# Kernel tuning notes

Measured on AMD Instinct MI355X. Metric: run time of the kernel, lower is better.

## Reference

```python
import jax, jax.numpy as jnp
import numpy as np

H = 8
D_MODEL = 1024
D_K = D_MODEL // H
NEG = -1000000000.0


def layer_norm(x, a, b, eps=1e-06):
    # torch std: unbiased (ddof=1); module divides by (std + eps)
    mean = jnp.mean(x, axis=-1, keepdims=True)
    var = jnp.sum((x - mean) ** 2, axis=-1, keepdims=True) / (x.shape[-1] - 1)
    std = jnp.sqrt(var)
    return a * (x - mean) / (std + eps) + b


def setup_inputs() -> dict:
    key = jax.random.key(0)
    ks = jax.random.split(key, 12)
    B, S, D = 8, 1024, D_MODEL
    inp = {
        "query": jax.random.normal(ks[0], (B, S, D), jnp.float32),
        "value": jax.random.normal(ks[1], (B, S, D), jnp.float32),
        "key": jax.random.normal(ks[2], (B, S, D), jnp.float32),
        "mask": jax.random.randint(ks[3], (B, S), 0, 2, jnp.int32),
        "ln_a": jnp.ones((D,), jnp.float32),
        "ln_b": jnp.zeros((D,), jnp.float32),
        "wq": jax.random.normal(ks[4], (D, D), jnp.float32) * 0.02,
        "bq": jnp.zeros((D,), jnp.float32),
        "wk": jax.random.normal(ks[5], (D, D), jnp.float32) * 0.02,
        "bk": jnp.zeros((D,), jnp.float32),
        "wv": jax.random.normal(ks[6], (D, D), jnp.float32) * 0.02,
        "bv": jnp.zeros((D,), jnp.float32),
        "w_aoa": jax.random.normal(ks[7], (2 * D, 2 * D), jnp.float32) * 0.02,  # [out, in]
        "b_aoa": jnp.zeros((2 * D,), jnp.float32),
    }
    return inp


def reference(query, value, key, mask, ln_a, ln_b, wq, bq, wk, bk, wv, bv, w_aoa, b_aoa):
    B, S, D = query.shape
    # mask [B,S] -> [B,1,1,S]
    m = mask[:, None, None, :]
    # norm_q
    q = layer_norm(query, ln_a, ln_b)
    # QKV projections, split heads -> [B,H,S,Dk]
    def split_heads(x):
        return x.reshape(B, -1, H, D_K).transpose(0, 2, 1, 3)
    q_ = split_heads(q @ wq.T + bq)
    k_ = split_heads(key @ wk.T + bk)
    v_ = split_heads(value @ wv.T + bv)
    scores = jnp.einsum("bhqd,bhkd->bhqk", q_, k_) / jnp.sqrt(jnp.float32(D_K))
    scores = jnp.where(m == 0, NEG, scores)
    p = jax.nn.softmax(scores, axis=-1)
    x = jnp.einsum("bhqk,bhkd->bhqd", p, v_)
    x = x.transpose(0, 2, 1, 3).reshape(B, S, D)
    # AoA: concat with (normed) query, linear to 2D, GLU
    z = jnp.concatenate([x, q], axis=-1) @ w_aoa.T + b_aoa
    a, g = jnp.split(z, 2, axis=-1)
    return a * jax.nn.sigmoid(g)
```

## Files before the change

### kernel.cpp

```cpp
#include <hip/hip_runtime.h>

typedef __attribute__((ext_vector_type(8))) __bf16 bf16x8;
typedef __attribute__((ext_vector_type(4))) float f32x4;

__device__ __forceinline__ ushort f2b(float f) {
    uint u = __builtin_bit_cast(uint, f);
    u += 0x7fffu + ((u >> 16) & 1u);
    return (ushort)(u >> 16);
}
__device__ __forceinline__ float b2f(ushort h) {
    uint u = ((uint)h) << 16;
    return __builtin_bit_cast(float, u);
}

__global__ __launch_bounds__(256) void cast_kernel(const float* __restrict__ src,
                                                   ushort* __restrict__ dst) {
    size_t i = ((size_t)blockIdx.x * 256 + threadIdx.x) * 4;
    float4 v = *(const float4*)(src + i);
    ushort4 o;
    o.x = f2b(v.x); o.y = f2b(v.y); o.z = f2b(v.z); o.w = f2b(v.w);
    *(ushort4*)(dst + i) = o;
}

__global__ __launch_bounds__(256) void cast_permute_aoa(const float* __restrict__ src,
                                                        ushort* __restrict__ dst) {
    int n1 = blockIdx.x >> 1;
    int c = (blockIdx.x & 1) * 1024 + threadIdx.x * 4;
    int q = ((n1 & 63) | ((n1 >> 7) << 6)) + ((n1 >> 6) & 1) * 1024;
    float4 v = *(const float4*)(src + (size_t)q * 2048 + c);
    ushort4 o;
    o.x = f2b(v.x); o.y = f2b(v.y); o.z = f2b(v.z); o.w = f2b(v.w);
    *(ushort4*)(dst + (size_t)n1 * 2048 + c) = o;
}

__global__ __launch_bounds__(256) void ln_kernel(const float* __restrict__ x,
                                                 const float* __restrict__ ga,
                                                 const float* __restrict__ be,
                                                 ushort* __restrict__ xq) {
    const int row = blockIdx.x, tid = threadIdx.x;
    __shared__ float red[4];
    float4 v = ((const float4*)(x + (size_t)row * 1024))[tid];
    float sm = v.x + v.y + v.z + v.w;
    for (int off = 32; off; off >>= 1) sm += __shfl_xor(sm, off);
    if ((tid & 63) == 0) red[tid >> 6] = sm;
    __syncthreads();
    float mean = (red[0] + red[1] + red[2] + red[3]) * (1.f / 1024.f);
    __syncthreads();
    float dx = v.x - mean, dy = v.y - mean, dz = v.z - mean, dw = v.w - mean;
    float s2 = dx * dx + dy * dy + dz * dz + dw * dw;
    for (int off = 32; off; off >>= 1) s2 += __shfl_xor(s2, off);
    if ((tid & 63) == 0) red[tid >> 6] = s2;
    __syncthreads();
    float var = (red[0] + red[1] + red[2] + red[3]) * (1.f / 1023.f);
    float inv = 1.f / (sqrtf(var) + 1e-6f);
    float4 g = ((const float4*)ga)[tid];
    float4 bb = ((const float4*)be)[tid];
    ushort4 o;
    o.x = f2b(g.x * dx * inv + bb.x);
    o.y = f2b(g.y * dy * inv + bb.y);
    o.z = f2b(g.z * dz * inv + bb.z);
    o.w = f2b(g.w * dw * inv + bb.w);
    *(ushort4*)&xq[(size_t)row * 2048 + 1024 + tid * 4] = o;
}

template <int MODE>
__global__ __launch_bounds__(512, 2) void gemm6(const ushort* __restrict__ Aq, int ldaq,
                                                const ushort* __restrict__ Ak,
                                                const ushort* __restrict__ Av,
                                                const ushort* __restrict__ B, int ldb,
                                                const float* __restrict__ bias0,
                                                const float* __restrict__ bias1,
                                                const float* __restrict__ bias2,
                                                void* __restrict__ out0,
                                                void* __restrict__ out1,
                                                void* __restrict__ out2,
                                                int K, int NB, float qscale) {
    __shared__ ushort lds[2][32768];

    const int tid = threadIdx.x;
    const int w = tid >> 6, l = tid & 63;
    const int wr = w >> 2, wcn = w & 3;
    const int r16 = l & 15, g4 = l >> 4;

    const int bid = blockIdx.x;
    const int cpx = gridDim.x >> 3;
    const int swz = (bid & 7) * cpx + (bid >> 3);
    const int m0 = (swz / NB) * 256;
    const int n0 = (swz % NB) * 256;

    const int region = (MODE == 0) ? (n0 >> 10) : 0;
    const ushort* A = (MODE == 0) ? (region == 0 ? Aq : (region == 1 ? Ak : Av)) : Aq;
    const int lda = (MODE == 0) ? (region == 0 ? ldaq : 1024) : ldaq;

    const int srow8 = l >> 3;
    const int sxor8 = ((l & 7) ^ srow8) * 8;
    const ushort* As0 = A + (size_t)(m0 + w * 8 + srow8) * lda + sxor8;
    const ushort* Bs0 = B + (size_t)(n0 + w * 8 + srow8) * ldb + sxor8;

    f32x4 acc[8][4];
#pragma unroll
    for (int i = 0; i < 8; i++)
#pragma unroll
        for (int j = 0; j < 4; j++) acc[i][j] = (f32x4){0.f, 0.f, 0.f, 0.f};

    const int sw16 = (r16 & 7) << 4;
    char* ldsb = (char*)&lds[0][0];

#define STAGE_H(sel_, HS_, kt_)                                                            \
    do {                                                                                   \
        const int mat_ = (HS_)&1, half_ = (HS_) >> 1;                                      \
        const ushort* sb_ = mat_ ? Bs0 : As0;                                              \
        const int ld_ = mat_ ? ldb : lda;                                                  \
        _Pragma("unroll") for (int li_ = 0; li_ < 2; li_++) {                              \
            const ushort* src_ = sb_ + (size_t)(half_ * 128 + li_ * 64) * ld_ + (kt_)*64;  \
            int dst_ = (sel_)*65536 + mat_ * 32768 + half_ * 16384 + li_ * 8192 + w * 1024;\
            __builtin_amdgcn_global_load_lds(                                              \
                (const __attribute__((address_space(1))) void*)src_,                       \
                (__attribute__((address_space(3))) void*)(ldsb + dst_), 16, 0, 0);         \
        }                                                                                  \
    } while (0)

    auto LDA4 = [&](bf16x8 (&dst)[4][2], int sel, int half) {
#pragma unroll
        for (int ai = 0; ai < 4; ai++)
#pragma unroll
            for (int ks = 0; ks < 2; ks++)
                dst[ai][ks] = *(const bf16x8*)(ldsb + sel * 65536 + half * 16384 +
                                               (wr * 16 + 32 * ai + r16) * 128 +
                                               ((ks * 64 + g4 * 16) ^ sw16));
    };
    auto LDB2 = [&](bf16x8 (&dst)[2][2], int sel, int half) {
#pragma unroll
        for (int bi = 0; bi < 2; bi++)
#pragma unroll
            for (int ks = 0; ks < 2; ks++)
                dst[bi][ks] = *(const bf16x8*)(ldsb + sel * 65536 + 32768 + half * 16384 +
                                               (wcn * 16 + 64 * bi + r16) * 128 +
                                               ((ks * 64 + g4 * 16) ^ sw16));
    };
    auto MM = [&](bf16x8 (&af)[4][2], bf16x8 (&bf)[2][2], int A0, int B0) {
        __builtin_amdgcn_s_setprio(1);
#pragma unroll
        for (int ks = 0; ks < 2; ks++)
#pragma unroll
            for (int ai = 0; ai < 4; ai++)
#pragma unroll
                for (int bi = 0; bi < 2; bi++)
                    acc[A0 + ai][B0 + bi] = __builtin_amdgcn_mfma_f32_16x16x32_bf16(
                        af[ai][ks], bf[bi][ks], acc[A0 + ai][B0 + bi], 0, 0, 0);
        __builtin_amdgcn_s_setprio(0);
    };

    const int NT = K >> 6;

    STAGE_H(0, 0, 0); STAGE_H(0, 1, 0); STAGE_H(0, 2, 0); STAGE_H(0, 3, 0);
    STAGE_H(1, 0, 1); STAGE_H(1, 1, 1); STAGE_H(1, 2, 1);
    asm volatile("s_waitcnt vmcnt(10)" ::: "memory");
    __builtin_amdgcn_s_barrier();

    bf16x8 aL[4][2], aH[4][2], bL[2][2], bH[2][2];

    for (int t = 0; t < NT - 2; ++t) {
        const int sel = t & 1;
        LDA4(aL, sel, 0); LDB2(bL, sel, 0);
        STAGE_H(sel ^ 1, 3, t + 1);
        __builtin_amdgcn_s_barrier();
        MM(aL, bL, 0, 0);
        asm volatile("s_waitcnt vmcnt(10)" ::: "memory");
        __builtin_amdgcn_s_barrier();
        LDA4(aH, sel, 1);
        STAGE_H(sel, 0, t + 2);
        __builtin_amdgcn_s_barrier();
        MM(aH, bL, 4, 0);
        asm volatile("s_waitcnt vmcnt(10)" ::: "memory");
        __builtin_amdgcn_s_barrier();
        LDB2(bH, sel, 1);
        STAGE_H(sel, 1, t + 2);
        __builtin_amdgcn_s_barrier();
        MM(aH, bH, 4, 2);
        __builtin_amdgcn_s_barrier();
        STAGE_H(sel, 2, t + 2);
        __builtin_amdgcn_s_barrier();
        MM(aL, bH, 0, 2);
        asm volatile("s_waitcnt vmcnt(10)" ::: "memory");
        __builtin_amdgcn_s_barrier();
    }
    {
        const int sel = (NT - 2) & 1;
        LDA4(aL, sel, 0); LDB2(bL, sel, 0);
        STAGE_H(sel ^ 1, 3, NT - 1);
        __builtin_amdgcn_s_barrier();
        MM(aL, bL, 0, 0);
        asm volatile("s_waitcnt vmcnt(10)" ::: "memory");
        __builtin_amdgcn_s_barrier();
        LDA4(aH, sel, 1);
        __builtin_amdgcn_s_barrier();
        MM(aH, bL, 4, 0);
        asm volatile("s_waitcnt vmcnt(8)" ::: "memory");
        __builtin_amdgcn_s_barrier();
        LDB2(bH, sel, 1);
        __builtin_amdgcn_s_barrier();
        MM(aH, bH, 4, 2);
        __builtin_amdgcn_s_barrier();
        MM(aL, bH, 0, 2);
        asm volatile("s_waitcnt vmcnt(4)" ::: "memory");
        __builtin_amdgcn_s_barrier();
    }
    {
        const int sel = (NT - 1) & 1;
        LDA4(aL, sel, 0); LDB2(bL, sel, 0);
        __builtin_amdgcn_s_barrier();
        MM(aL, bL, 0, 0);
        asm volatile("s_waitcnt vmcnt(2)" ::: "memory");
        __builtin_amdgcn_s_barrier();
        LDA4(aH, sel, 1);
        __builtin_amdgcn_s_barrier();
        MM(aH, bL, 4, 0);
        asm volatile("s_waitcnt vmcnt(0)" ::: "memory");
        __builtin_amdgcn_s_barrier();
        LDB2(bH, sel, 1);
        MM(aH, bH, 4, 2);
        MM(aL, bH, 0, 2);
    }
#undef STAGE_H

    if (MODE == 1) {
        float* out = (float*)out0;
#pragma unroll
        for (int bp = 0; bp < 2; bp++) {
            int j = (n0 >> 1) + wcn * 16 + 64 * bp + r16;
            float bsa = bias0[j];
            float bsg = bias0[j + 1024];
#pragma unroll
            for (int a_ = 0; a_ < 8; a_++) {
                int mr = m0 + wr * 16 + 32 * a_ + g4 * 4;
#pragma unroll
                for (int r = 0; r < 4; r++) {
                    float av = acc[a_][2 * bp][r] + bsa;
                    float gv = acc[a_][2 * bp + 1][r] + bsg;
                    out[(size_t)(mr + r) * 1024 + j] = av * (1.f / (1.f + __expf(-gv)));
                }
            }
        }
    } else {
        const int nr0 = n0 & 1023;
        const float* bias = region == 0 ? bias0 : (region == 1 ? bias1 : bias2);
        const float scale = region == 0 ? qscale : 1.f;
        if (region < 2) {
            ushort* C = (ushort*)(region == 0 ? out0 : out1);
#pragma unroll
            for (int b_ = 0; b_ < 4; b_++) {
                int n = nr0 + wcn * 16 + 64 * b_ + r16;
                float bs = bias[n];
#pragma unroll
                for (int a_ = 0; a_ < 8; a_++) {
                    int mr = m0 + wr * 16 + 32 * a_ + g4 * 4;
#pragma unroll
                    for (int r = 0; r < 4; r++)
                        C[(size_t)(mr + r) * 1024 + n] = f2b((acc[a_][b_][r] + bs) * scale);
                }
            }
        } else {
            ushort* Vt = (ushort*)out2;
#pragma unroll
            for (int b_ = 0; b_ < 4; b_++) {
                int n = nr0 + wcn * 16 + 64 * b_ + r16;
                float bs = bias[n];
                int h = n >> 7, d = n & 127;
#pragma unroll
                for (int a_ = 0; a_ < 8; a_++) {
                    int mr = m0 + wr * 16 + 32 * a_ + g4 * 4;
                    int bb = mr >> 10, s_ = mr & 1023;
                    ushort4 o;
                    o.x = f2b(acc[a_][b_][0] + bs);
                    o.y = f2b(acc[a_][b_][1] + bs);
                    o.z = f2b(acc[a_][b_][2] + bs);
                    o.w = f2b(acc[a_][b_][3] + bs);
                    *(ushort4*)&Vt[((size_t)(bb * 8 + h) * 128 + d) * 1024 + s_] = o;
                }
            }
        }
    }
}

__global__ __launch_bounds__(512, 4) void attn_kernel(const ushort* __restrict__ Q,
                                                      const ushort* __restrict__ Kt,
                                                      const ushort* __restrict__ Vt,
                                                      const int* __restrict__ mask,
                                                      ushort* __restrict__ xq) {
    __shared__ ushort Ks[2][8192];
    __shared__ ushort Vs[2][8192];
    __shared__ ushort Pl[8][1024];

    const int tid = threadIdx.x;
    const int l = tid & 63, wid = tid >> 6;
    const int r16 = l & 15, g4 = l >> 4;
    const int id = blockIdx.x;
    const int bh = ((id >> 6) << 3) | (id & 7);
    const int qb = (id >> 3) & 7;
    const int b = bh >> 3, h = bh & 7;
    const int q0 = qb * 128 + wid * 16;

    bf16x8 qf[4];
    const ushort* Qrow = Q + (size_t)(b * 1024 + q0 + r16) * 1024 + h * 128 + g4 * 8;
#pragma unroll
    for (int kf = 0; kf < 4; kf++) qf[kf] = *(const bf16x8*)(Qrow + kf * 32);

    const ushort* Kg = Kt + ((size_t)b * 1024) * 1024 + h * 128;
    const ushort* Vg = Vt + (size_t)(b * 8 + h) * 128 * 1024;
    const int* mptr = mask + b * 1024;

    f32x4 xacc[8];
#pragma unroll
    for (int i = 0; i < 8; i++) xacc[i] = (f32x4){0.f, 0.f, 0.f, 0.f};
    float mrow = -INFINITY, lrow = 0.f, sclp = 0.f;

    char* Pme = (char*)&Pl[wid][0];
    const int pswz = (r16 & 7) << 4;

    auto STAGE_K = [&](int sel, int t) {
        const int kv0 = t * 64;
#pragma unroll
        for (int it = 0; it < 2; ++it) {
            int ob = it * 8192 + wid * 1024;
            int o = ob + l * 16;
            int row = o >> 8;
            int sc = (o & 255) ^ ((row & 7) << 4);
            const ushort* src = Kg + (size_t)(kv0 + row) * 1024 + (sc >> 1);
            __builtin_amdgcn_global_load_lds((const __attribute__((address_space(1))) void*)src,
                (__attribute__((address_space(3))) void*)((char*)&Ks[sel][0] + ob), 16, 0, 0);
        }
    };
    auto STAGE_V = [&](int sel, int t) {
        const int kv0 = t * 64;
#pragma unroll
        for (int it = 0; it < 2; ++it) {
            int ob = it * 8192 + wid * 1024;
            int o = ob + l * 16;
            int d = o >> 7;
            int sc = (o & 127) ^ ((d & 7) << 4);
            const ushort* src = Vg + (size_t)d * 1024 + kv0 + (sc >> 1);
            __builtin_amdgcn_global_load_lds((const __attribute__((address_space(1))) void*)src,
                (__attribute__((address_space(3))) void*)((char*)&Vs[sel][0] + ob), 16, 0, 0);
        }
    };

    auto QK = [&](f32x4 (&s)[4], int sel, unsigned long long wt) {
        const char* Kb_ = (const char*)&Ks[sel][0];
#pragma unroll
        for (int cg = 0; cg < 4; cg++) {
            s[cg] = (f32x4){0.f, 0.f, 0.f, 0.f};
            const int rowk = cg * 16 + r16;
            const char* kr = Kb_ + rowk * 256;
            const int sw = (rowk & 7) << 4;
            __builtin_amdgcn_s_setprio(1);
#pragma unroll
            for (int kf = 0; kf < 4; kf++) {
                bf16x8 kfr = *(const bf16x8*)(kr + ((kf * 64 + g4 * 16) ^ sw));
                s[cg] = __builtin_amdgcn_mfma_f32_16x16x32_bf16(kfr, qf[kf], s[cg], 0, 0, 0);
            }
            __builtin_amdgcn_s_setprio(0);
            uint nib = (uint)(wt >> (cg * 16 + g4 * 4)) & 15u;
#pragma unroll
            for (int r = 0; r < 4; r++)
                if (!((nib >> r) & 1u)) s[cg][r] = -1e9f;
        }
    };
    auto PV = [&](int sel) {
        const char* Vb_ = (const char*)&Vs[sel][0];
        bf16x8 pfr[2];
#pragma unroll
        for (int ks = 0; ks < 2; ks++)
            pfr[ks] = *(const bf16x8*)(Pme + r16 * 128 + ((g4 * 16 + ks * 64) ^ pswz));
#pragma unroll
        for (int cg2 = 0; cg2 < 8; cg2++)
#pragma unroll
            for (int r = 0; r < 4; r++) xacc[cg2][r] *= sclp;
        __builtin_amdgcn_s_setprio(1);
#pragma unroll
        for (int ks = 0; ks < 2; ks++) {
#pragma unroll
            for (int cg2 = 0; cg2 < 8; cg2++) {
                const int d = cg2 * 16 + r16;
                bf16x8 vfr = *(const bf16x8*)(Vb_ + d * 128 + ((ks * 64 + g4 * 16) ^ ((d & 7) << 4)));
                xacc[cg2] = __builtin_amdgcn_mfma_f32_16x16x32_bf16(vfr, pfr[ks], xacc[cg2], 0, 0, 0);
            }
        }
        __builtin_amdgcn_s_setprio(0);
    };
    auto SOFTMAX = [&](f32x4 (&s)[4]) {
        float pmax = -INFINITY;
#pragma unroll
        for (int cg = 0; cg < 4; cg++)
#pragma unroll
            for (int r = 0; r < 4; r++) pmax = fmaxf(pmax, s[cg][r]);
        pmax = fmaxf(pmax, __shfl_xor(pmax, 16));
        pmax = fmaxf(pmax, __shfl_xor(pmax, 32));
        float mn = fmaxf(mrow, pmax);
        sclp = __expf(mrow - mn);
        mrow = mn;
        float rsum = 0.f;
#pragma unroll
        for (int cg = 0; cg < 4; cg++)
#pragma unroll
            for (int r = 0; r < 4; r++) {
                float p = __expf(s[cg][r] - mn);
                s[cg][r] = p;
                rsum += p;
            }
        rsum += __shfl_xor(rsum, 16);
        rsum += __shfl_xor(rsum, 32);
        lrow = lrow * sclp + rsum;
#pragma unroll
        for (int cg = 0; cg < 4; cg++) {
            uint lo = ((uint)f2b(s[cg][1]) << 16) | f2b(s[cg][0]);
            uint hi = ((uint)f2b(s[cg][3]) << 16) | f2b(s[cg][2]);
            uint2 pk; pk.x = lo; pk.y = hi;
            *(uint2*)(Pme + r16 * 128 + ((cg * 32 + g4 * 8) ^ pswz)) = pk;
        }
    };

    STAGE_K(0, 0);
    int mv = mptr[l];
    asm volatile("s_waitcnt vmcnt(0)" ::: "memory");
    __syncthreads();
    STAGE_K(1, 1);
    STAGE_V(0, 0);
    unsigned long long wt = __ballot(mv != 0);
    mv = mptr[64 + l];
    {
        f32x4 s0[4];
        QK(s0, 0, wt);
        SOFTMAX(s0);
    }
    int kc = 1, vc = 0;

    for (int u = 1; u < 16; ++u) {
        wt = __ballot(mv != 0);
        asm volatile("s_waitcnt vmcnt(0)" ::: "memory");
        __syncthreads();
        if (u < 15) STAGE_K(kc ^ 1, u + 1);
        STAGE_V(vc ^ 1, u);
        if (u < 15) mv = mptr[(u + 1) * 64 + l];

        f32x4 sn[4];
        QK(sn, kc, wt);
        PV(vc);
        SOFTMAX(sn);

        kc ^= 1; vc ^= 1;
    }

    asm volatile("s_waitcnt vmcnt(0)" ::: "memory");
    __syncthreads();
    PV(vc);

    const float inv = 1.f / lrow;
    const size_t orow = (size_t)(b * 1024 + q0 + r16) * 2048 + h * 128;
#pragma unroll
    for (int cg2 = 0; cg2 < 8; cg2++) {
#pragma unroll
        for (int r = 0; r < 4; r++) {
            xq[orow + cg2 * 16 + g4 * 4 + r] = f2b(xacc[cg2][r] * inv);
        }
    }
}

extern "C" void kernel_launch(void* const* d_in, const int* in_sizes, int n_in,
                              void* d_out, int out_size, void* d_ws, size_t ws_size,
                              hipStream_t stream) {
    const float* query = (const float*)d_in[0];
    const float* value = (const float*)d_in[1];
    const float* key   = (const float*)d_in[2];
    const int*   mask  = (const int*)d_in[3];
    const float* ln_a  = (const float*)d_in[4];
    const float* ln_b  = (const float*)d_in[5];
    const float* wq    = (const float*)d_in[6];
    const float* bq    = (const float*)d_in[7];
    const float* wk    = (const float*)d_in[8];
    const float* bk    = (const float*)d_in[9];
    const float* wv    = (const float*)d_in[10];
    const float* bv    = (const float*)d_in[11];
    const float* waoa  = (const float*)d_in[12];
    const float* baoa  = (const float*)d_in[13];
    float* out = (float*)d_out;

    char* w8 = (char*)d_ws;
    ushort* xq   = (ushort*)(w8);
    ushort* Qb   = (ushort*)(w8 + 33554432);
    ushort* Kb   = (ushort*)(w8 + 50331648);
    ushort* Vt   = (ushort*)(w8 + 67108864);
    ushort* keyb = (ushort*)(w8 + 83886080);
    ushort* valb = (ushort*)(w8 + 100663296);
    ushort* wqb  = (ushort*)(w8 + 117440512);
    ushort* wkb  = (ushort*)(w8 + 119537664);
    ushort* wvb  = (ushort*)(w8 + 121634816);
    ushort* wab  = (ushort*)(w8 + 123731968);

    cast_kernel<<<8192, 256, 0, stream>>>(key, keyb);
    cast_kernel<<<8192, 256, 0, stream>>>(value, valb);
    cast_kernel<<<1024, 256, 0, stream>>>(wq, wqb);
    cast_kernel<<<1024, 256, 0, stream>>>(wk, wkb);
    cast_kernel<<<1024, 256, 0, stream>>>(wv, wvb);
    cast_permute_aoa<<<4096, 256, 0, stream>>>(waoa, wab);
    ln_kernel<<<8192, 256, 0, stream>>>(query, ln_a, ln_b, xq);

    const float qscale = 0.08838834764831845f;

    gemm6<0><<<384, 512, 0, stream>>>(xq + 1024, 2048, keyb, valb,
                                      wqb, 1024, bq, bk, bv,
                                      Qb, Kb, Vt, 1024, 12, qscale);

    attn_kernel<<<512, 512, 0, stream>>>(Qb, Kb, Vt, mask, xq);

    gemm6<1><<<256, 512, 0, stream>>>(xq, 2048, nullptr, nullptr,
                                      wab, 2048, baoa, nullptr, nullptr,
                                      out, nullptr, nullptr, 2048, 8, 1.f);
}
```

Measured before the change: 236.3 us.

## Switch attention to 32x32x16 MFMA with 32 query rows per wave

Rewrites the attention kernel so each wave handles 32 query rows using 32x32x16 bf16 MFMA instructions instead of 16x16x32, doubling the queries per block and halving the grid to 256 blocks. Each staged K/V tile is reused across twice as many queries, which cuts LDS and global traffic per query and removes one cross-lane shuffle step in the softmax. Output stores are vectorized. In exchange register and LDS pressure rise (launch bounds drop to 2 blocks per SM), and 256 blocks may underfill the GPU's compute units.

```diff
diff --git a/kernel.cpp b/kernel.cpp
--- a/kernel.cpp
+++ b/kernel.cpp
@@ -2,6 +2,7 @@
 
 typedef __attribute__((ext_vector_type(8))) __bf16 bf16x8;
 typedef __attribute__((ext_vector_type(4))) float f32x4;
+typedef __attribute__((ext_vector_type(16))) float f32x16;
 
 __device__ __forceinline__ ushort f2b(float f) {
     uint u = __builtin_bit_cast(uint, f);
@@ -283,40 +284,42 @@
     }
 }
 
-__global__ __launch_bounds__(512, 4) void attn_kernel(const ushort* __restrict__ Q,
+__global__ __launch_bounds__(512, 2) void attn_kernel(const ushort* __restrict__ Q,
                                                       const ushort* __restrict__ Kt,
                                                       const ushort* __restrict__ Vt,
                                                       const int* __restrict__ mask,
                                                       ushort* __restrict__ xq) {
     __shared__ ushort Ks[2][8192];
     __shared__ ushort Vs[2][8192];
-    __shared__ ushort Pl[8][1024];
+    __shared__ ushort Pl[8][2048];
 
     const int tid = threadIdx.x;
     const int l = tid & 63, wid = tid >> 6;
-    const int r16 = l & 15, g4 = l >> 4;
+    const int ql = l & 31, hi = l >> 5;
     const int id = blockIdx.x;
-    const int bh = ((id >> 6) << 3) | (id & 7);
-    const int qb = (id >> 3) & 7;
+    const int bh = ((id >> 5) << 3) | (id & 7);
+    const int qb = (id >> 3) & 3;
     const int b = bh >> 3, h = bh & 7;
-    const int q0 = qb * 128 + wid * 16;
-
-    bf16x8 qf[4];
-    const ushort* Qrow = Q + (size_t)(b * 1024 + q0 + r16) * 1024 + h * 128 + g4 * 8;
-#pragma unroll
-    for (int kf = 0; kf < 4; kf++) qf[kf] = *(const bf16x8*)(Qrow + kf * 32);
+    const int q0 = qb * 256 + wid * 32;
+
+    bf16x8 qf[8];
+    const ushort* Qrow = Q + (size_t)(b * 1024 + q0 + ql) * 1024 + h * 128 + hi * 8;
+#pragma unroll
+    for (int ks = 0; ks < 8; ks++) qf[ks] = *(const bf16x8*)(Qrow + ks * 16);
 
     const ushort* Kg = Kt + ((size_t)b * 1024) * 1024 + h * 128;
     const ushort* Vg = Vt + (size_t)(b * 8 + h) * 128 * 1024;
     const int* mptr = mask + b * 1024;
 
-    f32x4 xacc[8];
-#pragma unroll
-    for (int i = 0; i < 8; i++) xacc[i] = (f32x4){0.f, 0.f, 0.f, 0.f};
+    f32x16 xacc[4];
+#pragma unroll
+    for (int i = 0; i < 4; i++)
+#pragma unroll
+        for (int r = 0; r < 16; r++) xacc[i][r] = 0.f;
     float mrow = -INFINITY, lrow = 0.f, sclp = 0.f;
 
     char* Pme = (char*)&Pl[wid][0];
-    const int pswz = (r16 & 7) << 4;
+    const int pswz = (ql & 7) << 4;
 
     auto STAGE_K = [&](int sel, int t) {
         const int kv0 = t * 64;
@@ -345,79 +348,83 @@
         }
     };
 
-    auto QK = [&](f32x4 (&s)[4], int sel, unsigned long long wt) {
+    auto QK = [&](f32x16 (&s)[2], int sel, unsigned long long wt) {
         const char* Kb_ = (const char*)&Ks[sel][0];
 #pragma unroll
-        for (int cg = 0; cg < 4; cg++) {
-            s[cg] = (f32x4){0.f, 0.f, 0.f, 0.f};
-            const int rowk = cg * 16 + r16;
+        for (int sub = 0; sub < 2; sub++) {
+            f32x16 sacc;
+#pragma unroll
+            for (int r = 0; r < 16; r++) sacc[r] = 0.f;
+            const int rowk = sub * 32 + ql;
             const char* kr = Kb_ + rowk * 256;
             const int sw = (rowk & 7) << 4;
             __builtin_amdgcn_s_setprio(1);
 #pragma unroll
-            for (int kf = 0; kf < 4; kf++) {
-                bf16x8 kfr = *(const bf16x8*)(kr + ((kf * 64 + g4 * 16) ^ sw));
-                s[cg] = __builtin_amdgcn_mfma_f32_16x16x32_bf16(kfr, qf[kf], s[cg], 0, 0, 0);
+            for (int ks = 0; ks < 8; ks++) {
+                bf16x8 kfr = *(const bf16x8*)(kr + ((ks * 32 + hi * 16) ^ sw));
+                sacc = __builtin_amdgcn_mfma_f32_32x32x16_bf16(kfr, qf[ks], sacc, 0, 0, 0);
             }
             __builtin_amdgcn_s_setprio(0);
-            uint nib = (uint)(wt >> (cg * 16 + g4 * 4)) & 15u;
-#pragma unroll
-            for (int r = 0; r < 4; r++)
-                if (!((nib >> r) & 1u)) s[cg][r] = -1e9f;
+#pragma unroll
+            for (int q2 = 0; q2 < 4; q2++) {
+                uint nib = (uint)(wt >> (8 * q2 + 4 * hi + 32 * sub)) & 15u;
+#pragma unroll
+                for (int r = 0; r < 4; r++)
+                    if (!((nib >> r) & 1u)) sacc[4 * q2 + r] = -1e9f;
+            }
+            s[sub] = sacc;
         }
     };
     auto PV = [&](int sel) {
         const char* Vb_ = (const char*)&Vs[sel][0];
-        bf16x8 pfr[2];
-#pragma unroll
-        for (int ks = 0; ks < 2; ks++)
-            pfr[ks] = *(const bf16x8*)(Pme + r16 * 128 + ((g4 * 16 + ks * 64) ^ pswz));
-#pragma unroll
-        for (int cg2 = 0; cg2 < 8; cg2++)
-#pragma unroll
-            for (int r = 0; r < 4; r++) xacc[cg2][r] *= sclp;
-        __builtin_amdgcn_s_setprio(1);
-#pragma unroll
-        for (int ks = 0; ks < 2; ks++) {
-#pragma unroll
-            for (int cg2 = 0; cg2 < 8; cg2++) {
-                const int d = cg2 * 16 + r16;
-                bf16x8 vfr = *(const bf16x8*)(Vb_ + d * 128 + ((ks * 64 + g4 * 16) ^ ((d & 7) << 4)));
-                xacc[cg2] = __builtin_amdgcn_mfma_f32_16x16x32_bf16(vfr, pfr[ks], xacc[cg2], 0, 0, 0);
-            }
-        }
-        __builtin_amdgcn_s_setprio(0);
-    };
-    auto SOFTMAX = [&](f32x4 (&s)[4]) {
+        const int vsw = (ql & 7) << 4;
+#pragma unroll
+        for (int df = 0; df < 4; df++)
+#pragma unroll
+            for (int r = 0; r < 16; r++) xacc[df][r] *= sclp;
+#pragma unroll
+        for (int ks2 = 0; ks2 < 4; ks2++) {
+            bf16x8 pfr = *(const bf16x8*)(Pme + ql * 128 + ((ks2 * 32 + hi * 16) ^ pswz));
+            __builtin_amdgcn_s_setprio(1);
+#pragma unroll
+            for (int df = 0; df < 4; df++) {
+                const int d = df * 32 + ql;
+                bf16x8 vfr = *(const bf16x8*)(Vb_ + d * 128 + ((ks2 * 32 + hi * 16) ^ vsw));
+                xacc[df] = __builtin_amdgcn_mfma_f32_32x32x16_bf16(vfr, pfr, xacc[df], 0, 0, 0);
+            }
+            __builtin_amdgcn_s_setprio(0);
+        }
+    };
+    auto SOFTMAX = [&](f32x16 (&s)[2]) {
         float pmax = -INFINITY;
 #pragma unroll
-        for (int cg = 0; cg < 4; cg++)
-#pragma unroll
-            for (int r = 0; r < 4; r++) pmax = fmaxf(pmax, s[cg][r]);
-        pmax = fmaxf(pmax, __shfl_xor(pmax, 16));
+        for (int res = 0; res < 2; res++)
+#pragma unroll
+            for (int r = 0; r < 16; r++) pmax = fmaxf(pmax, s[res][r]);
         pmax = fmaxf(pmax, __shfl_xor(pmax, 32));
         float mn = fmaxf(mrow, pmax);
         sclp = __expf(mrow - mn);
         mrow = mn;
         float rsum = 0.f;
 #pragma unroll
-        for (int cg = 0; cg < 4; cg++)
-#pragma unroll
-            for (int r = 0; r < 4; r++) {
-                float p = __expf(s[cg][r] - mn);
-                s[cg][r] = p;
+        for (int res = 0; res < 2; res++)
+#pragma unroll
+            for (int r = 0; r < 16; r++) {
+                float p = __expf(s[res][r] - mn);
+                s[res][r] = p;
                 rsum += p;
             }
-        rsum += __shfl_xor(rsum, 16);
         rsum += __shfl_xor(rsum, 32);
         lrow = lrow * sclp + rsum;
 #pragma unroll
-        for (int cg = 0; cg < 4; cg++) {
-            uint lo = ((uint)f2b(s[cg][1]) << 16) | f2b(s[cg][0]);
-            uint hi = ((uint)f2b(s[cg][3]) << 16) | f2b(s[cg][2]);
-            uint2 pk; pk.x = lo; pk.y = hi;
-            *(uint2*)(Pme + r16 * 128 + ((cg * 32 + g4 * 8) ^ pswz)) = pk;
-        }
+        for (int res = 0; res < 2; res++)
+#pragma unroll
+            for (int q2 = 0; q2 < 4; q2++) {
+                uint lo = ((uint)f2b(s[res][4 * q2 + 1]) << 16) | f2b(s[res][4 * q2]);
+                uint hi2 = ((uint)f2b(s[res][4 * q2 + 3]) << 16) | f2b(s[res][4 * q2 + 2]);
+                uint2 pk; pk.x = lo; pk.y = hi2;
+                *(uint2*)(Pme + ql * 128 + ((16 * q2 + 8 * hi + 64 * res) ^ pswz)) = pk;
+            }
     };
 
     STAGE_K(0, 0);
@@ -428,11 +435,9 @@
     STAGE_V(0, 0);
     unsigned long long wt = __ballot(mv != 0);
     mv = mptr[64 + l];
-    {
-        f32x4 s0[4];
-        QK(s0, 0, wt);
-        SOFTMAX(s0);
-    }
+    f32x16 s[2];
+    QK(s, 0, wt);
+    SOFTMAX(s);
     int kc = 1, vc = 0;
 
     for (int u = 1; u < 16; ++u) {
@@ -443,10 +448,9 @@
         STAGE_V(vc ^ 1, u);
         if (u < 15) mv = mptr[(u + 1) * 64 + l];
 
-        f32x4 sn[4];
-        QK(sn, kc, wt);
+        QK(s, kc, wt);
         PV(vc);
-        SOFTMAX(sn);
+        SOFTMAX(s);
 
         kc ^= 1; vc ^= 1;
     }
@@ -456,12 +460,17 @@
     PV(vc);
 
     const float inv = 1.f / lrow;
-    const size_t orow = (size_t)(b * 1024 + q0 + r16) * 2048 + h * 128;
-#pragma unroll
-    for (int cg2 = 0; cg2 < 8; cg2++) {
-#pragma unroll
-        for (int r = 0; r < 4; r++) {
-            xq[orow + cg2 * 16 + g4 * 4 + r] = f2b(xacc[cg2][r] * inv);
+    const size_t orow = (size_t)(b * 1024 + q0 + ql) * 2048 + h * 128;
+#pragma unroll
+    for (int df = 0; df < 4; df++) {
+#pragma unroll
+        for (int q2 = 0; q2 < 4; q2++) {
+            ushort4 o;
+            o.x = f2b(xacc[df][4 * q2 + 0] * inv);
+            o.y = f2b(xacc[df][4 * q2 + 1] * inv);
+            o.z = f2b(xacc[df][4 * q2 + 2] * inv);
+            o.w = f2b(xacc[df][4 * q2 + 3] * inv);
+            *(ushort4*)&xq[orow + df * 32 + 8 * q2 + 4 * hi] = o;
         }
     }
 }
@@ -511,7 +520,7 @@
                                       wqb, 1024, bq, bk, bv,
                                       Qb, Kb, Vt, 1024, 12, qscale);
 
-    attn_kernel<<<512, 512, 0, stream>>>(Qb, Kb, Vt, mask, xq);
+    attn_kernel<<<256, 512, 0, stream>>>(Qb, Kb, Vt, mask, xq);
 
     gemm6<1><<<256, 512, 0, stream>>>(xq, 2048, nullptr, nullptr,
                                       wab, 2048, baoa, nullptr, nullptr,
```

After: 239.5 us. No clear change (+1.3%).
